# Optimization experiments

Measured on AMD Instinct MI355X. Metric: run time of the kernel, lower is better.

## Reference

```python
import jax, jax.numpy as jnp
import numpy as np

EPS = 1e-6

def _ln(x):
    # LayerNorm, no affine, eps=1e-6
    mu = jnp.mean(x, axis=-1, keepdims=True)
    var = jnp.mean((x - mu) ** 2, axis=-1, keepdims=True)
    return (x - mu) / jnp.sqrt(var + EPS)

def _attend(q, k, v, mask_add, scale):
    # q,k,v: [B,H,N,D]; mask_add: [B,1,1,N]
    attn = jnp.einsum('bhqd,bhkd->bhqk', q, k) * scale + mask_add
    attn = jax.nn.softmax(attn, axis=-1)
    return jnp.einsum('bhqk,bhkd->bhqd', attn, v)

def setup_inputs() -> dict:
    key = jax.random.key(0)
    ks = jax.random.split(key, 16)
    B, N, C, H = 4, 1024, 1024, 16
    mlp_h = 4 * C
    s = 0.02
    inp = {
        'x': jax.random.normal(ks[0], (B, N, C), jnp.float32),
        'c': jax.random.normal(ks[1], (B, N, C), jnp.float32),
        'mask': jax.random.randint(ks[2], (B, N), 0, 2, jnp.int32),
        # self-attention params
        'sa_qkv_w': jax.random.normal(ks[3], (C, 3 * C), jnp.float32) * s,
        'sa_qkv_b': jnp.zeros((3 * C,), jnp.float32),
        'sa_proj_w': jax.random.normal(ks[4], (C, C), jnp.float32) * s,
        'sa_proj_b': jnp.zeros((C,), jnp.float32),
        # cross-attention params
        'ca_q_w': jax.random.normal(ks[5], (C, C), jnp.float32) * s,
        'ca_q_b': jnp.zeros((C,), jnp.float32),
        'ca_k_w': jax.random.normal(ks[6], (C, C), jnp.float32) * s,
        'ca_k_b': jnp.zeros((C,), jnp.float32),
        'ca_v_w': jax.random.normal(ks[7], (C, C), jnp.float32) * s,
        'ca_v_b': jnp.zeros((C,), jnp.float32),
        'ca_proj_w': jax.random.normal(ks[8], (C, C), jnp.float32) * s,
        'ca_proj_b': jnp.zeros((C,), jnp.float32),
        # MLP params
        'fc1_w': jax.random.normal(ks[9], (C, mlp_h), jnp.float32) * s,
        'fc1_b': jnp.zeros((mlp_h,), jnp.float32),
        'fc2_w': jax.random.normal(ks[10], (mlp_h, C), jnp.float32) * s,
        'fc2_b': jnp.zeros((C,), jnp.float32),
    }
    return inp

def reference(x, c, mask,
              sa_qkv_w, sa_qkv_b, sa_proj_w, sa_proj_b,
              ca_q_w, ca_q_b, ca_k_w, ca_k_b, ca_v_w, ca_v_b, ca_proj_w, ca_proj_b,
              fc1_w, fc1_b, fc2_w, fc2_b):
    B, N, C = x.shape
    H = 16
    D = C // H
    scale = D ** -0.5
    # additive mask: 0 where mask==1, -10000 elsewhere; [B,1,1,N]
    mask_add = jnp.where(mask[:, None, None, :] != 1, -10000.0, 0.0).astype(jnp.float32)

    def split_heads(t):  # [B,N,C] -> [B,H,N,D]
        return t.reshape(B, N, H, D).transpose(0, 2, 1, 3)

    # self-attention
    h = _ln(x)
    qkv = h @ sa_qkv_w + sa_qkv_b  # [B,N,3C]
    q, k, v = (split_heads(t) for t in jnp.split(qkv, 3, axis=-1))
    sa = _attend(q, k, v, mask_add, scale).transpose(0, 2, 1, 3).reshape(B, N, C)
    x = x + sa @ sa_proj_w + sa_proj_b

    # cross-attention
    h = _ln(x)
    q = split_heads(h @ ca_q_w + ca_q_b)
    k = split_heads(c @ ca_k_w + ca_k_b)
    v = split_heads(c @ ca_v_w + ca_v_b)
    ca = _attend(q, k, v, mask_add, scale).transpose(0, 2, 1, 3).reshape(B, N, C)
    x = x + ca @ ca_proj_w + ca_proj_b

    # MLP with exact (erf) GELU, matching nn.GELU() default
    h = _ln(x)
    h = jax.nn.gelu(h @ fc1_w + fc1_b, approximate=False)
    x = x + h @ fc2_w + fc2_b
    return x
```

## Files before the change

kernel.cpp:

```cpp
#include <hip/hip_runtime.h>
#include <hip/hip_bf16.h>
#include <cstdint>

typedef __bf16 bf16;
typedef __bf16 b8v __attribute__((ext_vector_type(8)));
typedef __bf16 b4v __attribute__((ext_vector_type(4)));
typedef float  f32x4 __attribute__((ext_vector_type(4)));

#define MFMA16(a, b, c) __builtin_amdgcn_mfma_f32_16x16x32_bf16((a), (b), (c), 0, 0, 0)

__device__ inline void gload_lds16(const void* g, void* l) {
    __builtin_amdgcn_global_load_lds(
        (const __attribute__((address_space(1))) void*)g,
        (__attribute__((address_space(3))) void*)l, 16, 0, 0);
}

__global__ __launch_bounds__(256) void f32_to_bf16_k(const float* __restrict__ in,
                                                     bf16* __restrict__ out) {
    long i = ((long)blockIdx.x * 256 + threadIdx.x) * 8;
    float4 f0 = *(const float4*)&in[i];
    float4 f1 = *(const float4*)&in[i + 4];
    b8v v;
    v[0] = (bf16)f0.x; v[1] = (bf16)f0.y; v[2] = (bf16)f0.z; v[3] = (bf16)f0.w;
    v[4] = (bf16)f1.x; v[5] = (bf16)f1.y; v[6] = (bf16)f1.z; v[7] = (bf16)f1.w;
    *(b8v*)&out[i] = v;
}

__global__ __launch_bounds__(256) void transpose_w_k(const float* __restrict__ in,
                                                     bf16* __restrict__ out,
                                                     int K, int N) {
    __shared__ bf16 t[64][66];
    const int tn = blockIdx.x * 64, tk = blockIdx.y * 64;
    const int tid = threadIdx.x;
    const int r = tid >> 4, c4 = (tid & 15) * 4;
#pragma unroll
    for (int rr = r; rr < 64; rr += 16) {
        float4 v = *(const float4*)&in[(long)(tk + rr) * N + tn + c4];
        *(ushort2*)&t[rr][c4]     = ushort2{ ((ushort2*)&v.x)[0].x ? 0 : 0, 0 };
        t[rr][c4 + 0] = (bf16)v.x;
        t[rr][c4 + 1] = (bf16)v.y;
        t[rr][c4 + 2] = (bf16)v.z;
        t[rr][c4 + 3] = (bf16)v.w;
    }
    __syncthreads();
    const int n = tid >> 3, k8 = (tid & 7) * 8;
#pragma unroll
    for (int nn = n; nn < 64; nn += 32) {
        b8v v;
#pragma unroll
        for (int j = 0; j < 8; ++j) v[j] = t[k8 + j][nn];
        *(b8v*)&out[(long)(tn + nn) * K + tk + k8] = v;
    }
}

__global__ __launch_bounds__(256) void layernorm_k(const float* __restrict__ x,
                                                   bf16* __restrict__ h) {
    int row = blockIdx.x;
    const float* xr = x + (long)row * 1024;
    int tid = threadIdx.x;
    float4 v = ((const float4*)xr)[tid];
    float s = v.x + v.y + v.z + v.w;
    float ss = v.x * v.x + v.y * v.y + v.z * v.z + v.w * v.w;
    for (int m = 1; m < 64; m <<= 1) {
        s += __shfl_xor(s, m);
        ss += __shfl_xor(ss, m);
    }
    __shared__ float sbuf[8];
    int wave = tid >> 6, lane = tid & 63;
    if (lane == 0) { sbuf[wave] = s; sbuf[4 + wave] = ss; }
    __syncthreads();
    s = sbuf[0] + sbuf[1] + sbuf[2] + sbuf[3];
    ss = sbuf[4] + sbuf[5] + sbuf[6] + sbuf[7];
    float mu = s * (1.0f / 1024.0f);
    float var = ss * (1.0f / 1024.0f) - mu * mu;
    float rstd = rsqrtf(var + 1e-6f);
    b4v o;
    o[0] = (bf16)((v.x - mu) * rstd);
    o[1] = (bf16)((v.y - mu) * rstd);
    o[2] = (bf16)((v.z - mu) * rstd);
    o[3] = (bf16)((v.w - mu) * rstd);
    *(b4v*)&h[(long)row * 1024 + tid * 4] = o;
}

template <int EPI, int WM>
__global__ __launch_bounds__(256, 2) void gemm_bt(const bf16* __restrict__ A,
                                                  const bf16* __restrict__ Bt,
                                                  const float* __restrict__ bias,
                                                  const float* __restrict__ bias2,
                                                  int nsplit,
                                                  bf16* __restrict__ outb,
                                                  float* __restrict__ res,
                                                  int M, int N, int K) {
    constexpr int BM = WM * 32;
    __shared__ __align__(16) bf16 As[BM * 32];
    __shared__ __align__(16) bf16 Bs[128 * 32];
    const int tid = threadIdx.x;
    const int wave = tid >> 6, lane = tid & 63;
    const int quad = lane >> 4, l16 = lane & 15;
    const int bm = blockIdx.y, bn = blockIdx.x;
    const int wm = wave >> 1, wn = wave & 1;

    f32x4 acc[WM][4] = {};
    const long Abase = (long)bm * BM * K;
    const long Bbase = (long)bn * 128 * K;

    for (int k0 = 0; k0 < K; k0 += 32) {
        __syncthreads();
#pragma unroll
        for (int it = 0; it < BM / 64; ++it) {
            int chunk = it * 256 + tid;
            int row = chunk >> 2, col = (chunk & 3) << 3;
            gload_lds16(A + Abase + (long)row * K + k0 + col,
                        (char*)As + it * 4096 + wave * 1024);
        }
#pragma unroll
        for (int it = 0; it < 2; ++it) {
            int chunk = it * 256 + tid;
            int row = chunk >> 2, col = (chunk & 3) << 3;
            gload_lds16(Bt + Bbase + (long)row * K + k0 + col,
                        (char*)Bs + it * 4096 + wave * 1024);
        }
        __syncthreads();
        b8v a[WM], b[4];
#pragma unroll
        for (int i = 0; i < WM; ++i)
            a[i] = *(const b8v*)&As[(wm * WM * 16 + i * 16 + l16) * 32 + quad * 8];
#pragma unroll
        for (int i = 0; i < 4; ++i)
            b[i] = *(const b8v*)&Bs[(wn * 64 + i * 16 + l16) * 32 + quad * 8];
#pragma unroll
        for (int im = 0; im < WM; ++im)
#pragma unroll
            for (int in = 0; in < 4; ++in)
                acc[im][in] = MFMA16(a[im], b[in], acc[im][in]);
    }

    const int rbase = bm * BM + wm * WM * 16;
    const int cbase = bn * 128 + wn * 64;
#pragma unroll
    for (int in = 0; in < 4; ++in) {
        int col = cbase + in * 16 + l16;
        float bv = (col < nsplit) ? bias[col] : bias2[col - nsplit];
#pragma unroll
        for (int im = 0; im < WM; ++im) {
            int row0 = rbase + im * 16 + quad * 4;
#pragma unroll
            for (int r = 0; r < 4; ++r) {
                long off = (long)(row0 + r) * N + col;
                float v = acc[im][in][r] + bv;
                if (EPI == 0) {
                    outb[off] = (bf16)v;
                } else if (EPI == 1) {
                    res[off] += v;
                } else {
                    v = 0.5f * v * (1.0f + erff(v * 0.70710678118654752f));
                    outb[off] = (bf16)v;
                }
            }
        }
    }
}

__global__ __launch_bounds__(256) void attn_k(const bf16* __restrict__ qp, int qs,
                                              const bf16* __restrict__ kp, int ks,
                                              const bf16* __restrict__ vp, int vs,
                                              const int* __restrict__ mask,
                                              bf16* __restrict__ outp) {
    const int bh = blockIdx.y;
    const int b = bh >> 4, hidx = bh & 15;
    const int qt = blockIdx.x;
    const int tid = threadIdx.x;
    const int wave = tid >> 6, lane = tid & 63;
    const int quad = lane >> 4, l16 = lane & 15;

    __shared__ __align__(16) bf16 Qs[64 * 64];
    __shared__ __align__(16) bf16 Ks[64 * 64];
    __shared__ __align__(16) bf16 Vt[64 * 72];
    __shared__ __align__(16) bf16 Ps[4][16 * 64];

    const int hoff = hidx * 64;
    const long rowbase = (long)b * 1024;

    for (int i = tid; i < 512; i += 256) {
        int rr = i >> 3, cc = (i & 7) << 3;
        *(b8v*)&Qs[rr * 64 + cc] = *(const b8v*)&qp[(rowbase + qt * 64 + rr) * qs + hoff + cc];
    }
    __syncthreads();
    b8v qf[2];
    qf[0] = *(const b8v*)&Qs[(wave * 16 + l16) * 64 + quad * 8];
    qf[1] = *(const b8v*)&Qs[(wave * 16 + l16) * 64 + 32 + quad * 8];

    float m_i[4], l_i[4];
    f32x4 o[4] = {};
    for (int r = 0; r < 4; ++r) { m_i[r] = -1e30f; l_i[r] = 0.0f; }
    const float scale = 0.125f;

    for (int kt = 0; kt < 16; ++kt) {
        __syncthreads();
        for (int i = tid; i < 512; i += 256) {
            int rr = i >> 3, cc = (i & 7) << 3;
            *(b8v*)&Ks[rr * 64 + cc] = *(const b8v*)&kp[(rowbase + kt * 64 + rr) * ks + hoff + cc];
            b8v vv = *(const b8v*)&vp[(rowbase + kt * 64 + rr) * vs + hoff + cc];
            for (int j = 0; j < 8; ++j) Vt[(cc + j) * 72 + rr] = vv[j];
        }
        __syncthreads();

        float sv[4][4];
        float rowmax[4] = {-1e30f, -1e30f, -1e30f, -1e30f};
        for (int f = 0; f < 4; ++f) {
            f32x4 acc = {};
            b8v kf0 = *(const b8v*)&Ks[(f * 16 + l16) * 64 + quad * 8];
            b8v kf1 = *(const b8v*)&Ks[(f * 16 + l16) * 64 + 32 + quad * 8];
            acc = MFMA16(qf[0], kf0, acc);
            acc = MFMA16(qf[1], kf1, acc);
            int key = kt * 64 + f * 16 + l16;
            float madd = (mask[b * 1024 + key] != 1) ? -10000.0f : 0.0f;
            for (int r = 0; r < 4; ++r) {
                float s = acc[r] * scale + madd;
                sv[f][r] = s;
                rowmax[r] = fmaxf(rowmax[r], s);
            }
        }
        for (int m = 1; m < 16; m <<= 1)
            for (int r = 0; r < 4; ++r) rowmax[r] = fmaxf(rowmax[r], __shfl_xor(rowmax[r], m));

        float alpha[4], rowsum[4];
        for (int r = 0; r < 4; ++r) {
            float mnew = fmaxf(m_i[r], rowmax[r]);
            alpha[r] = __expf(m_i[r] - mnew);
            m_i[r] = mnew;
            rowsum[r] = 0.0f;
        }
        for (int f = 0; f < 4; ++f)
            for (int r = 0; r < 4; ++r) {
                float p = __expf(sv[f][r] - m_i[r]);
                sv[f][r] = p;
                rowsum[r] += p;
            }
        for (int m = 1; m < 16; m <<= 1)
            for (int r = 0; r < 4; ++r) rowsum[r] += __shfl_xor(rowsum[r], m);
        for (int r = 0; r < 4; ++r) l_i[r] = l_i[r] * alpha[r] + rowsum[r];

        for (int f = 0; f < 4; ++f)
            for (int r = 0; r < 4; ++r)
                Ps[wave][(quad * 4 + r) * 64 + f * 16 + l16] = (bf16)sv[f][r];
        b8v pf0 = *(const b8v*)&Ps[wave][l16 * 64 + quad * 8];
        b8v pf1 = *(const b8v*)&Ps[wave][l16 * 64 + 32 + quad * 8];

        for (int f = 0; f < 4; ++f) {
            f32x4 t = o[f];
            for (int r = 0; r < 4; ++r) t[r] *= alpha[r];
            b8v vf0 = *(const b8v*)&Vt[(f * 16 + l16) * 72 + quad * 8];
            b8v vf1 = *(const b8v*)&Vt[(f * 16 + l16) * 72 + 32 + quad * 8];
            t = MFMA16(pf0, vf0, t);
            t = MFMA16(pf1, vf1, t);
            o[f] = t;
        }
    }

    for (int f = 0; f < 4; ++f)
        for (int r = 0; r < 4; ++r) {
            int row = qt * 64 + wave * 16 + quad * 4 + r;
            int col = hoff + f * 16 + l16;
            outp[(rowbase + row) * 1024 + col] = (bf16)(o[f][r] / l_i[r]);
        }
}

extern "C" void kernel_launch(void* const* d_in, const int* in_sizes, int n_in,
                              void* d_out, int out_size, void* d_ws, size_t ws_size,
                              hipStream_t stream) {
    const float* x = (const float*)d_in[0];
    const float* c = (const float*)d_in[1];
    const int* mask = (const int*)d_in[2];
    const float* qkv_w = (const float*)d_in[3];
    const float* qkv_b = (const float*)d_in[4];
    const float* sap_w = (const float*)d_in[5];
    const float* sap_b = (const float*)d_in[6];
    const float* caq_w = (const float*)d_in[7], *caq_b = (const float*)d_in[8];
    const float* cak_w = (const float*)d_in[9], *cak_b = (const float*)d_in[10];
    const float* cav_w = (const float*)d_in[11], *cav_b = (const float*)d_in[12];
    const float* cap_w = (const float*)d_in[13], *cap_b = (const float*)d_in[14];
    const float* fc1_w = (const float*)d_in[15], *fc1_b = (const float*)d_in[16];
    const float* fc2_w = (const float*)d_in[17], *fc2_b = (const float*)d_in[18];

    float* xf = (float*)d_out;

    char* ws = (char*)d_ws;
    bf16* wT = (bf16*)ws;
    bf16* qkvT = wT;
    bf16* sapT = wT + 3145728;
    bf16* caqT = wT + 4194304;
    bf16* cakvT = wT + 5242880;
    bf16* capT = wT + 7340032;
    bf16* fc1T = wT + 8388608;
    bf16* fc2T = wT + 12582912;
    bf16* h    = (bf16*)(ws + (32L << 20));
    bf16* att  = (bf16*)(ws + (40L << 20));
    bf16* qkv  = (bf16*)(ws + (48L << 20));
    bf16* q2   = (bf16*)(ws + (48L << 20));
    bf16* k2v2 = (bf16*)(ws + (56L << 20));
    bf16* gel  = (bf16*)(ws + (48L << 20));
    bf16* cbf  = (bf16*)(ws + (72L << 20));

    transpose_w_k<<<dim3(48, 16), 256, 0, stream>>>(qkv_w, qkvT, 1024, 3072);
    transpose_w_k<<<dim3(16, 16), 256, 0, stream>>>(sap_w, sapT, 1024, 1024);
    transpose_w_k<<<dim3(16, 16), 256, 0, stream>>>(caq_w, caqT, 1024, 1024);
    transpose_w_k<<<dim3(16, 16), 256, 0, stream>>>(cak_w, cakvT, 1024, 1024);
    transpose_w_k<<<dim3(16, 16), 256, 0, stream>>>(cav_w, cakvT + 1048576, 1024, 1024);
    transpose_w_k<<<dim3(16, 16), 256, 0, stream>>>(cap_w, capT, 1024, 1024);
    transpose_w_k<<<dim3(64, 16), 256, 0, stream>>>(fc1_w, fc1T, 1024, 4096);
    transpose_w_k<<<dim3(16, 64), 256, 0, stream>>>(fc2_w, fc2T, 4096, 1024);

    f32_to_bf16_k<<<2048, 256, 0, stream>>>(c, cbf);
    hipMemcpyAsync(xf, x, 4096L * 1024 * 4, hipMemcpyDeviceToDevice, stream);

    layernorm_k<<<4096, 256, 0, stream>>>(xf, h);
    gemm_bt<0, 4><<<dim3(24, 32), 256, 0, stream>>>(h, qkvT, qkv_b, qkv_b, 3072, qkv, nullptr, 4096, 3072, 1024);
    attn_k<<<dim3(16, 64), 256, 0, stream>>>(qkv, 3072, qkv + 1024, 3072, qkv + 2048, 3072, mask, att);
    gemm_bt<1, 2><<<dim3(8, 64), 256, 0, stream>>>(att, sapT, sap_b, sap_b, 1024, nullptr, xf, 4096, 1024, 1024);

    layernorm_k<<<4096, 256, 0, stream>>>(xf, h);
    gemm_bt<0, 2><<<dim3(8, 64), 256, 0, stream>>>(h, caqT, caq_b, caq_b, 1024, q2, nullptr, 4096, 1024, 1024);
    gemm_bt<0, 4><<<dim3(16, 32), 256, 0, stream>>>(cbf, cakvT, cak_b, cav_b, 1024, k2v2, nullptr, 4096, 2048, 1024);
    attn_k<<<dim3(16, 64), 256, 0, stream>>>(q2, 1024, k2v2, 2048, k2v2 + 1024, 2048, mask, att);
    gemm_bt<1, 2><<<dim3(8, 64), 256, 0, stream>>>(att, capT, cap_b, cap_b, 1024, nullptr, xf, 4096, 1024, 1024);

    layernorm_k<<<4096, 256, 0, stream>>>(xf, h);
    gemm_bt<2, 4><<<dim3(32, 32), 256, 0, stream>>>(h, fc1T, fc1_b, fc1_b, 4096, gel, nullptr, 4096, 4096, 1024);
    gemm_bt<1, 2><<<dim3(8, 64), 256, 0, stream>>>(gel, fc2T, fc2_b, fc2_b, 1024, nullptr, xf, 4096, 1024, 4096);
}
```

Baseline: 644.5 us.

## Pre-transpose V per head and cache mask in LDS for attention

Adds a separate kernel that writes V in head-major transposed layout, so the attention kernel loads V tiles with vectorized 16-byte copies instead of scattering scalar transposed stores into shared memory. The additive mask for all keys is precomputed once per block into shared memory rather than read from global memory in every inner iteration. The P scratch buffer stride is padded to 72 to reduce LDS bank conflicts, and the inner loops are explicitly unrolled. The trade-off is an extra kernel launch plus a round trip of V through global memory for each attention call, reusing the h buffer as scratch.

```diff
diff --git a/kernel.cpp b/kernel.cpp
--- a/kernel.cpp
+++ b/kernel.cpp
@@ -36,7 +36,6 @@
 #pragma unroll
     for (int rr = r; rr < 64; rr += 16) {
         float4 v = *(const float4*)&in[(long)(tk + rr) * N + tn + c4];
-        *(ushort2*)&t[rr][c4]     = ushort2{ ((ushort2*)&v.x)[0].x ? 0 : 0, 0 };
         t[rr][c4 + 0] = (bf16)v.x;
         t[rr][c4 + 1] = (bf16)v.y;
         t[rr][c4 + 2] = (bf16)v.z;
@@ -50,6 +49,34 @@
 #pragma unroll
         for (int j = 0; j < 8; ++j) v[j] = t[k8 + j][nn];
         *(b8v*)&out[(long)(tn + nn) * K + tk + k8] = v;
+    }
+}
+
+__global__ __launch_bounds__(256) void transpose_v_k(const bf16* __restrict__ vp, int vs,
+                                                     bf16* __restrict__ VT) {
+    __shared__ bf16 t[64][66];
+    const int bh = blockIdx.y;
+    const long rowbase = (long)(bh >> 4) * 1024;
+    const int hoff = (bh & 15) * 64;
+    const int tk = blockIdx.x * 64;
+    const int tid = threadIdx.x;
+    const int r = tid >> 4, c4 = (tid & 15) * 4;
+#pragma unroll
+    for (int rr = r; rr < 64; rr += 16) {
+        b4v v = *(const b4v*)&vp[(rowbase + tk + rr) * vs + hoff + c4];
+        t[rr][c4 + 0] = v[0];
+        t[rr][c4 + 1] = v[1];
+        t[rr][c4 + 2] = v[2];
+        t[rr][c4 + 3] = v[3];
+    }
+    __syncthreads();
+    const int d = tid >> 3, k8 = (tid & 7) * 8;
+#pragma unroll
+    for (int dd = d; dd < 64; dd += 32) {
+        b8v v;
+#pragma unroll
+        for (int j = 0; j < 8; ++j) v[j] = t[k8 + j][dd];
+        *(b8v*)&VT[((long)bh * 64 + dd) * 1024 + tk + k8] = v;
     }
 }
 
@@ -163,7 +190,7 @@
 
 __global__ __launch_bounds__(256) void attn_k(const bf16* __restrict__ qp, int qs,
                                               const bf16* __restrict__ kp, int ks,
-                                              const bf16* __restrict__ vp, int vs,
+                                              const bf16* __restrict__ VT,
                                               const int* __restrict__ mask,
                                               bf16* __restrict__ outp) {
     const int bh = blockIdx.y;
@@ -175,12 +202,22 @@
 
     __shared__ __align__(16) bf16 Qs[64 * 64];
     __shared__ __align__(16) bf16 Ks[64 * 64];
-    __shared__ __align__(16) bf16 Vt[64 * 72];
-    __shared__ __align__(16) bf16 Ps[4][16 * 64];
+    __shared__ __align__(16) bf16 Vs[64 * 72];
+    __shared__ __align__(16) bf16 Ps[4][16 * 72];
+    __shared__ float madd_s[1024];
 
     const int hoff = hidx * 64;
     const long rowbase = (long)b * 1024;
 
+    {
+        int4 mv = *(const int4*)&mask[b * 1024 + tid * 4];
+        float4 mf;
+        mf.x = (mv.x != 1) ? -10000.0f : 0.0f;
+        mf.y = (mv.y != 1) ? -10000.0f : 0.0f;
+        mf.z = (mv.z != 1) ? -10000.0f : 0.0f;
+        mf.w = (mv.w != 1) ? -10000.0f : 0.0f;
+        *(float4*)&madd_s[tid * 4] = mf;
+    }
     for (int i = tid; i < 512; i += 256) {
         int rr = i >> 3, cc = (i & 7) << 3;
         *(b8v*)&Qs[rr * 64 + cc] = *(const b8v*)&qp[(rowbase + qt * 64 + rr) * qs + hoff + cc];
@@ -200,65 +237,79 @@
         for (int i = tid; i < 512; i += 256) {
             int rr = i >> 3, cc = (i & 7) << 3;
             *(b8v*)&Ks[rr * 64 + cc] = *(const b8v*)&kp[(rowbase + kt * 64 + rr) * ks + hoff + cc];
-            b8v vv = *(const b8v*)&vp[(rowbase + kt * 64 + rr) * vs + hoff + cc];
-            for (int j = 0; j < 8; ++j) Vt[(cc + j) * 72 + rr] = vv[j];
+            *(b8v*)&Vs[rr * 72 + cc] = *(const b8v*)&VT[((long)bh * 64 + rr) * 1024 + kt * 64 + cc];
         }
         __syncthreads();
 
         float sv[4][4];
         float rowmax[4] = {-1e30f, -1e30f, -1e30f, -1e30f};
+#pragma unroll
         for (int f = 0; f < 4; ++f) {
             f32x4 acc = {};
             b8v kf0 = *(const b8v*)&Ks[(f * 16 + l16) * 64 + quad * 8];
             b8v kf1 = *(const b8v*)&Ks[(f * 16 + l16) * 64 + 32 + quad * 8];
             acc = MFMA16(qf[0], kf0, acc);
             acc = MFMA16(qf[1], kf1, acc);
-            int key = kt * 64 + f * 16 + l16;
-            float madd = (mask[b * 1024 + key] != 1) ? -10000.0f : 0.0f;
+            float madd = madd_s[kt * 64 + f * 16 + l16];
+#pragma unroll
             for (int r = 0; r < 4; ++r) {
                 float s = acc[r] * scale + madd;
                 sv[f][r] = s;
                 rowmax[r] = fmaxf(rowmax[r], s);
             }
         }
+#pragma unroll
         for (int m = 1; m < 16; m <<= 1)
+#pragma unroll
             for (int r = 0; r < 4; ++r) rowmax[r] = fmaxf(rowmax[r], __shfl_xor(rowmax[r], m));
 
         float alpha[4], rowsum[4];
+#pragma unroll
         for (int r = 0; r < 4; ++r) {
             float mnew = fmaxf(m_i[r], rowmax[r]);
             alpha[r] = __expf(m_i[r] - mnew);
             m_i[r] = mnew;
             rowsum[r] = 0.0f;
         }
+#pragma unroll
         for (int f = 0; f < 4; ++f)
+#pragma unroll
             for (int r = 0; r < 4; ++r) {
                 float p = __expf(sv[f][r] - m_i[r]);
                 sv[f][r] = p;
                 rowsum[r] += p;
             }
+#pragma unroll
         for (int m = 1; m < 16; m <<= 1)
+#pragma unroll
             for (int r = 0; r < 4; ++r) rowsum[r] += __shfl_xor(rowsum[r], m);
+#pragma unroll
         for (int r = 0; r < 4; ++r) l_i[r] = l_i[r] * alpha[r] + rowsum[r];
 
+#pragma unroll
         for (int f = 0; f < 4; ++f)
+#pragma unroll
             for (int r = 0; r < 4; ++r)
-                Ps[wave][(quad * 4 + r) * 64 + f * 16 + l16] = (bf16)sv[f][r];
-        b8v pf0 = *(const b8v*)&Ps[wave][l16 * 64 + quad * 8];
-        b8v pf1 = *(const b8v*)&Ps[wave][l16 * 64 + 32 + quad * 8];
-
+                Ps[wave][(quad * 4 + r) * 72 + f * 16 + l16] = (bf16)sv[f][r];
+        b8v pf0 = *(const b8v*)&Ps[wave][l16 * 72 + quad * 8];
+        b8v pf1 = *(const b8v*)&Ps[wave][l16 * 72 + 32 + quad * 8];
+
+#pragma unroll
         for (int f = 0; f < 4; ++f) {
             f32x4 t = o[f];
+#pragma unroll
             for (int r = 0; r < 4; ++r) t[r] *= alpha[r];
-            b8v vf0 = *(const b8v*)&Vt[(f * 16 + l16) * 72 + quad * 8];
-            b8v vf1 = *(const b8v*)&Vt[(f * 16 + l16) * 72 + 32 + quad * 8];
+            b8v vf0 = *(const b8v*)&Vs[(f * 16 + l16) * 72 + quad * 8];
+            b8v vf1 = *(const b8v*)&Vs[(f * 16 + l16) * 72 + 32 + quad * 8];
             t = MFMA16(pf0, vf0, t);
             t = MFMA16(pf1, vf1, t);
             o[f] = t;
         }
     }
 
+#pragma unroll
     for (int f = 0; f < 4; ++f)
+#pragma unroll
         for (int r = 0; r < 4; ++r) {
             int row = qt * 64 + wave * 16 + quad * 4 + r;
             int col = hoff + f * 16 + l16;
@@ -295,6 +346,7 @@
     bf16* fc1T = wT + 8388608;
     bf16* fc2T = wT + 12582912;
     bf16* h    = (bf16*)(ws + (32L << 20));
+    bf16* VT   = h;
     bf16* att  = (bf16*)(ws + (40L << 20));
     bf16* qkv  = (bf16*)(ws + (48L << 20));
     bf16* q2   = (bf16*)(ws + (48L << 20));
@@ -316,13 +368,15 @@
 
     layernorm_k<<<4096, 256, 0, stream>>>(xf, h);
     gemm_bt<0, 4><<<dim3(24, 32), 256, 0, stream>>>(h, qkvT, qkv_b, qkv_b, 3072, qkv, nullptr, 4096, 3072, 1024);
-    attn_k<<<dim3(16, 64), 256, 0, stream>>>(qkv, 3072, qkv + 1024, 3072, qkv + 2048, 3072, mask, att);
+    transpose_v_k<<<dim3(16, 64), 256, 0, stream>>>(qkv + 2048, 3072, VT);
+    attn_k<<<dim3(16, 64), 256, 0, stream>>>(qkv, 3072, qkv + 1024, 3072, VT, mask, att);
     gemm_bt<1, 2><<<dim3(8, 64), 256, 0, stream>>>(att, sapT, sap_b, sap_b, 1024, nullptr, xf, 4096, 1024, 1024);
 
     layernorm_k<<<4096, 256, 0, stream>>>(xf, h);
     gemm_bt<0, 2><<<dim3(8, 64), 256, 0, stream>>>(h, caqT, caq_b, caq_b, 1024, q2, nullptr, 4096, 1024, 1024);
     gemm_bt<0, 4><<<dim3(16, 32), 256, 0, stream>>>(cbf, cakvT, cak_b, cav_b, 1024, k2v2, nullptr, 4096, 2048, 1024);
-    attn_k<<<dim3(16, 64), 256, 0, stream>>>(q2, 1024, k2v2, 2048, k2v2 + 1024, 2048, mask, att);
+    transpose_v_k<<<dim3(16, 64), 256, 0, stream>>>(k2v2 + 1024, 2048, VT);
+    attn_k<<<dim3(16, 64), 256, 0, stream>>>(q2, 1024, k2v2, 2048, VT, mask, att);
     gemm_bt<1, 2><<<dim3(8, 64), 256, 0, stream>>>(att, capT, cap_b, cap_b, 1024, nullptr, xf, 4096, 1024, 1024);
 
     layernorm_k<<<4096, 256, 0, stream>>>(xf, h);
```

After: 606.2 us. 1.06x faster.
